# Kernel tuning notes

Hardware: AMD Instinct MI355X
Metric: run time of the kernel (lower is better)

Reference implementation:

```python
import jax, jax.numpy as jnp
import numpy as np

N, C, H, W = 2, 8, 256, 512
K = 9   # kernel_size
D = 1   # dilation


def setup_inputs() -> dict:
    key = jax.random.key(0)
    k1, k2, k3 = jax.random.split(key, 3)
    x_in = jax.random.normal(k1, (N, C, H, W), dtype=jnp.float32)
    filters = jax.random.normal(k2, (N, K * K, H, W), dtype=jnp.float32)
    filters_biases = jax.random.normal(k3, (N, 1, H, W), dtype=jnp.float32)
    return {"x_in": x_in, "filters": filters, "filters_biases": filters_biases}


def reference(x_in, filters, filters_biases):
    # Dynamic (per-pixel) filtering: out[n,c,h,w] = sum_{i,j} x_pad[n,c,h+i*d,w+j*d] * filters[n,i*K+j,h,w] + bias
    # Equivalent to torch: unfold -> [N,C,K*K,H,W], multiply by filters [N,1,K*K,H,W], sum over K*K, add bias.
    # Fused accumulation over the K*K taps avoids materializing the K*K-times larger im2col tensor.
    k, d = K, D
    p = d * (k - 1) // 2  # 'same' padding used by im2col_layer
    n, c, h, w = x_in.shape
    xp = jnp.pad(x_in, ((0, 0), (0, 0), (p, p), (p, p)))
    out = jnp.zeros_like(x_in)
    for i in range(k):          # fixed small kernel loop (81 taps), unrolled by jit
        for j in range(k):
            tap = filters[:, None, i * k + j]                  # [N,1,H,W]
            out = out + xp[:, :, i * d:i * d + h, j * d:j * d + w] * tap
    return out + filters_biases
```

## Files before the change

### kernel.cpp

```cpp
#include <hip/hip_runtime.h>

#define CC 8
#define HH 256
#define WW 512
#define KK 9
#define XS_STRIDE 532

__global__ __launch_bounds__(256) void dynfilter_kernel(
    const float* __restrict__ x,
    const float* __restrict__ filt,
    const float* __restrict__ fbias,
    float* __restrict__ out)
{
    __shared__ __align__(16) float xs[CC][XS_STRIDE];

    const int tid = threadIdx.x;
    const int bid = blockIdx.x;
    const int n = bid >> 8;
    const int h = bid & 255;
    const int w0 = tid << 1;

    const int lane32 = tid & 31;
    const int cstage = tid >> 5;

    float acc0[CC], acc1[CC];
    {
        const float2 fb = *(const float2*)(fbias + (n * HH + h) * WW + w0);
        #pragma unroll
        for (int c = 0; c < CC; ++c) { acc0[c] = fb.x; acc1[c] = fb.y; }
    }

    const float* xcbase = x + ((size_t)(n * CC + cstage)) * HH * WW;

    for (int i = 0; i < KK; ++i) {
        const int hh = h + i - 4;
        const bool rowok = (hh >= 0) && (hh < HH);

        __syncthreads();
        const float4* src = (const float4*)(xcbase + hh * WW);
        #pragma unroll
        for (int it = 0; it < 5; ++it) {
            const int k = lane32 + (it << 5);
            if (k < 130) {
                const int w = (k << 2) - 4;
                float4 v = make_float4(0.f, 0.f, 0.f, 0.f);
                if (rowok && (unsigned)w < (unsigned)WW) v = src[w >> 2];
                *(float4*)&xs[cstage][w + 4] = v;
            }
        }
        __syncthreads();

        const float* frow = filt + ((size_t)(n * 81 + i * KK) * HH + h) * WW + w0;
        float2 fr[KK];
        #pragma unroll
        for (int j = 0; j < KK; ++j)
            fr[j] = *(const float2*)(frow + (size_t)j * (HH * WW));

        #pragma unroll
        for (int c = 0; c < CC; ++c) {
            float xr[10];
            #pragma unroll
            for (int s = 0; s < 5; ++s)
                *(float2*)&xr[2 * s] = *(const float2*)&xs[c][w0 + 2 * s];
            #pragma unroll
            for (int j = 0; j < KK; ++j) {
                acc0[c] = fmaf(fr[j].x, xr[j],     acc0[c]);
                acc1[c] = fmaf(fr[j].y, xr[j + 1], acc1[c]);
            }
        }
    }

    #pragma unroll
    for (int c = 0; c < CC; ++c) {
        *(float2*)(out + ((size_t)(n * CC + c) * HH + h) * WW + w0) =
            make_float2(acc0[c], acc1[c]);
    }
}

extern "C" void kernel_launch(void* const* d_in, const int* in_sizes, int n_in,
                              void* d_out, int out_size, void* d_ws, size_t ws_size,
                              hipStream_t stream) {
    const float* x  = (const float*)d_in[0];
    const float* f  = (const float*)d_in[1];
    const float* fb = (const float*)d_in[2];
    float* o = (float*)d_out;
    hipLaunchKernelGGL(dynfilter_kernel, dim3(2 * HH), dim3(256), 0, stream,
                       x, f, fb, o);
}
```

Baseline: 156.3 us.

## Split rows into segments, remap threads to pixels×channel-pairs, double-buffer LDS

Each image row is now split into two 256-pixel segments, which doubles the grid. Each thread now computes 4 pixels for 2 channels instead of 2 pixels for 8 channels. The input rows are double-buffered in shared memory, and the next tap row is prefetched into registers while the current one is being computed, so each tap row needs a single barrier. The aim is more blocks in flight and load latency hidden behind FMAs. The cost is that each filter value is now loaded by four channel-pair thread groups instead of one, which adds cache traffic.

```diff
diff --git a/kernel.cpp b/kernel.cpp
--- a/kernel.cpp
+++ b/kernel.cpp
@@ -4,76 +4,104 @@
 #define HH 256
 #define WW 512
 #define KK 9
-#define XS_STRIDE 532
+#define SEGW 256
+#define XF 272
 
-__global__ __launch_bounds__(256) void dynfilter_kernel(
+__global__ __launch_bounds__(256, 4) void dynfilter_kernel(
     const float* __restrict__ x,
     const float* __restrict__ filt,
     const float* __restrict__ fbias,
     float* __restrict__ out)
 {
-    __shared__ __align__(16) float xs[CC][XS_STRIDE];
+    __shared__ __align__(16) float xs[2][CC][XF];
 
     const int tid = threadIdx.x;
     const int bid = blockIdx.x;
-    const int n = bid >> 8;
-    const int h = bid & 255;
-    const int w0 = tid << 1;
+    const int seg = bid & 1;
+    const int h   = (bid >> 1) & 255;
+    const int n   = bid >> 9;
+
+    const int pxg = tid & 63;
+    const int cp  = tid >> 6;
+    const int w0  = seg * SEGW + (pxg << 2);
+    const int c0  = cp << 1;
 
     const int lane32 = tid & 31;
     const int cstage = tid >> 5;
+    const float* xrowbase = x + ((size_t)(n * CC + cstage)) * (HH * WW)
+                              + (seg * SEGW - 8);
+    const int wbase = seg * SEGW - 8;
 
-    float acc0[CC], acc1[CC];
+    float acc[2][4];
     {
-        const float2 fb = *(const float2*)(fbias + (n * HH + h) * WW + w0);
+        const float4 fb = *(const float4*)(fbias + ((size_t)(n * HH + h)) * WW + w0);
         #pragma unroll
-        for (int c = 0; c < CC; ++c) { acc0[c] = fb.x; acc1[c] = fb.y; }
-    }
-
-    const float* xcbase = x + ((size_t)(n * CC + cstage)) * HH * WW;
-
-    for (int i = 0; i < KK; ++i) {
-        const int hh = h + i - 4;
-        const bool rowok = (hh >= 0) && (hh < HH);
-
-        __syncthreads();
-        const float4* src = (const float4*)(xcbase + hh * WW);
-        #pragma unroll
-        for (int it = 0; it < 5; ++it) {
-            const int k = lane32 + (it << 5);
-            if (k < 130) {
-                const int w = (k << 2) - 4;
-                float4 v = make_float4(0.f, 0.f, 0.f, 0.f);
-                if (rowok && (unsigned)w < (unsigned)WW) v = src[w >> 2];
-                *(float4*)&xs[cstage][w + 4] = v;
-            }
-        }
-        __syncthreads();
-
-        const float* frow = filt + ((size_t)(n * 81 + i * KK) * HH + h) * WW + w0;
-        float2 fr[KK];
-        #pragma unroll
-        for (int j = 0; j < KK; ++j)
-            fr[j] = *(const float2*)(frow + (size_t)j * (HH * WW));
-
-        #pragma unroll
-        for (int c = 0; c < CC; ++c) {
-            float xr[10];
-            #pragma unroll
-            for (int s = 0; s < 5; ++s)
-                *(float2*)&xr[2 * s] = *(const float2*)&xs[c][w0 + 2 * s];
-            #pragma unroll
-            for (int j = 0; j < KK; ++j) {
-                acc0[c] = fmaf(fr[j].x, xr[j],     acc0[c]);
-                acc1[c] = fmaf(fr[j].y, xr[j + 1], acc1[c]);
-            }
+        for (int cc = 0; cc < 2; ++cc) {
+            acc[cc][0] = fb.x; acc[cc][1] = fb.y; acc[cc][2] = fb.z; acc[cc][3] = fb.w;
         }
     }
 
+    float4 xv[3];
+    auto issue_stage = [&](int hh) {
+        const bool rowok = (unsigned)hh < (unsigned)HH;
+        const float* src = xrowbase + (size_t)hh * WW;
+        #pragma unroll
+        for (int r = 0; r < 3; ++r) {
+            const int k = lane32 + (r << 5);
+            const int wg = wbase + (k << 2);
+            xv[r] = make_float4(0.f, 0.f, 0.f, 0.f);
+            if (k < 68 && rowok && (unsigned)wg < (unsigned)WW)
+                xv[r] = *(const float4*)(src + (k << 2));
+        }
+    };
+    auto store_stage = [&](int buf) {
+        #pragma unroll
+        for (int r = 0; r < 3; ++r) {
+            const int k = lane32 + (r << 5);
+            if (k < 68) *(float4*)&xs[buf][cstage][k << 2] = xv[r];
+        }
+    };
+
+    issue_stage(h - 4);
+    store_stage(0);
+    __syncthreads();
+
+    const size_t HW = (size_t)HH * WW;
+    const float* fbase = filt + ((size_t)(n * 81) * HH + h) * WW + w0;
+
     #pragma unroll
-    for (int c = 0; c < CC; ++c) {
-        *(float2*)(out + ((size_t)(n * CC + c) * HH + h) * WW + w0) =
-            make_float2(acc0[c], acc1[c]);
+    for (int i = 0; i < KK; ++i) {
+        float4 fr[KK];
+        #pragma unroll
+        for (int j = 0; j < KK; ++j)
+            fr[j] = *(const float4*)(fbase + (size_t)(i * KK + j) * HW);
+
+        if (i < KK - 1) issue_stage(h - 4 + i + 1);
+
+        #pragma unroll
+        for (int cc = 0; cc < 2; ++cc) {
+            const float* xr = &xs[i & 1][c0 + cc][(pxg << 2) + 4];
+            float xf[12];
+            *(float4*)&xf[0] = *(const float4*)&xr[0];
+            *(float4*)&xf[4] = *(const float4*)&xr[4];
+            *(float4*)&xf[8] = *(const float4*)&xr[8];
+            #pragma unroll
+            for (int j = 0; j < KK; ++j) {
+                acc[cc][0] = fmaf(fr[j].x, xf[j],     acc[cc][0]);
+                acc[cc][1] = fmaf(fr[j].y, xf[j + 1], acc[cc][1]);
+                acc[cc][2] = fmaf(fr[j].z, xf[j + 2], acc[cc][2]);
+                acc[cc][3] = fmaf(fr[j].w, xf[j + 3], acc[cc][3]);
+            }
+        }
+
+        if (i < KK - 1) store_stage((i + 1) & 1);
+        __syncthreads();
+    }
+
+    #pragma unroll
+    for (int cc = 0; cc < 2; ++cc) {
+        *(float4*)(out + ((size_t)(n * CC + c0 + cc) * HH + h) * WW + w0) =
+            make_float4(acc[cc][0], acc[cc][1], acc[cc][2], acc[cc][3]);
     }
 }
 
@@ -84,6 +112,6 @@
     const float* f  = (const float*)d_in[1];
     const float* fb = (const float*)d_in[2];
     float* o = (float*)d_out;
-    hipLaunchKernelGGL(dynfilter_kernel, dim3(2 * HH), dim3(256), 0, stream,
+    hipLaunchKernelGGL(dynfilter_kernel, dim3(2 * HH * 2), dim3(256), 0, stream,
                        x, f, fb, o);
 }
```

Measured after the change: 382.1 us. 144% more time.

## Split rows into half-width segments, split channels across threads, double-buffer LDS rows

Applied to the files above, without the earlier changes.

Each block now covers half a row: 1024 blocks instead of 512, and each thread computes 4 channels for 2 pixels instead of 8 channels. The x row staging is double-buffered in shared memory, so the next row's global loads are issued before the FMAs on the current row, and there is one barrier per tap row instead of two. The goal is more parallelism and occupancy, plus overlap of load latency with compute. The cost is that filter taps are now loaded twice per pixel, once for each channel group, and each block stages some redundant halo.

```diff
diff --git a/kernel.cpp b/kernel.cpp
--- a/kernel.cpp
+++ b/kernel.cpp
@@ -4,76 +4,111 @@
 #define HH 256
 #define WW 512
 #define KK 9
-#define XS_STRIDE 532
+#define XF 268
 
-__global__ __launch_bounds__(256) void dynfilter_kernel(
+__global__ __launch_bounds__(256, 4) void dynfilter_kernel(
     const float* __restrict__ x,
     const float* __restrict__ filt,
     const float* __restrict__ fbias,
     float* __restrict__ out)
 {
-    __shared__ __align__(16) float xs[CC][XS_STRIDE];
+    __shared__ __align__(16) float xs[2][CC][XF];
 
     const int tid = threadIdx.x;
     const int bid = blockIdx.x;
-    const int n = bid >> 8;
-    const int h = bid & 255;
-    const int w0 = tid << 1;
+    const int seg = bid & 1;
+    const int h   = (bid >> 1) & 255;
+    const int n   = bid >> 9;
 
-    const int lane32 = tid & 31;
-    const int cstage = tid >> 5;
+    const int pxg = tid & 127;
+    const int cg  = tid >> 7;
+    const int w0  = seg * 256 + (pxg << 1);
 
-    float acc0[CC], acc1[CC];
+    const int lane32  = tid & 31;
+    const int cstage  = tid >> 5;
+    const int wstage0 = seg * 256 - 4;
+    const float* xcrow = x + ((size_t)(n * CC + cstage)) * ((size_t)HH * WW) + wstage0;
+
+    const size_t HW = (size_t)HH * WW;
+    const float* fbase = filt + ((size_t)(n * 81) * HH + h) * WW + w0;
+
+    float acc[4][2];
     {
-        const float2 fb = *(const float2*)(fbias + (n * HH + h) * WW + w0);
+        const float2 fb = *(const float2*)(fbias + ((size_t)(n * HH + h)) * WW + w0);
         #pragma unroll
-        for (int c = 0; c < CC; ++c) { acc0[c] = fb.x; acc1[c] = fb.y; }
+        for (int c = 0; c < 4; ++c) { acc[c][0] = fb.x; acc[c][1] = fb.y; }
     }
 
-    const float* xcbase = x + ((size_t)(n * CC + cstage)) * HH * WW;
+    {
+        const int hh = h - 4;
+        const bool rowok = (hh >= 0);
+        const float* src = xcrow + (size_t)hh * WW;
+        float4 s0 = make_float4(0.f,0.f,0.f,0.f), s1 = s0, s2 = s0;
+        int w;
+        w = wstage0 + (lane32 << 2);
+        if (rowok && (unsigned)w < (unsigned)WW) s0 = *(const float4*)(src + (lane32 << 2));
+        w = wstage0 + ((lane32 + 32) << 2);
+        if (rowok && (unsigned)w < (unsigned)WW) s1 = *(const float4*)(src + ((lane32 + 32) << 2));
+        w = wstage0 + ((lane32 + 64) << 2);
+        if (lane32 < 2 && rowok && (unsigned)w < (unsigned)WW) s2 = *(const float4*)(src + ((lane32 + 64) << 2));
+        *(float4*)&xs[0][cstage][lane32 << 2] = s0;
+        *(float4*)&xs[0][cstage][(lane32 + 32) << 2] = s1;
+        if (lane32 < 2) *(float4*)&xs[0][cstage][(lane32 + 64) << 2] = s2;
+    }
+    __syncthreads();
 
+    #pragma unroll
     for (int i = 0; i < KK; ++i) {
-        const int hh = h + i - 4;
-        const bool rowok = (hh >= 0) && (hh < HH);
+        const int buf = i & 1;
 
-        __syncthreads();
-        const float4* src = (const float4*)(xcbase + hh * WW);
+        float2 f[KK];
         #pragma unroll
-        for (int it = 0; it < 5; ++it) {
-            const int k = lane32 + (it << 5);
-            if (k < 130) {
-                const int w = (k << 2) - 4;
-                float4 v = make_float4(0.f, 0.f, 0.f, 0.f);
-                if (rowok && (unsigned)w < (unsigned)WW) v = src[w >> 2];
-                *(float4*)&xs[cstage][w + 4] = v;
+        for (int j = 0; j < KK; ++j)
+            f[j] = *(const float2*)(fbase + (size_t)(i * KK + j) * HW);
+
+        float4 s0 = make_float4(0.f,0.f,0.f,0.f), s1 = s0, s2 = s0;
+        if (i < KK - 1) {
+            const int hh = h - 4 + i + 1;
+            const bool rowok = (unsigned)hh < (unsigned)HH;
+            const float* src = xcrow + (size_t)hh * WW;
+            int w;
+            w = wstage0 + (lane32 << 2);
+            if (rowok && (unsigned)w < (unsigned)WW) s0 = *(const float4*)(src + (lane32 << 2));
+            w = wstage0 + ((lane32 + 32) << 2);
+            if (rowok && (unsigned)w < (unsigned)WW) s1 = *(const float4*)(src + ((lane32 + 32) << 2));
+            w = wstage0 + ((lane32 + 64) << 2);
+            if (lane32 < 2 && rowok && (unsigned)w < (unsigned)WW) s2 = *(const float4*)(src + ((lane32 + 64) << 2));
+        }
+
+        #pragma unroll
+        for (int c = 0; c < 4; ++c) {
+            const float* xp = &xs[buf][(cg << 2) + c][pxg << 1];
+            float xr[10];
+            float2 v;
+            v = *(const float2*)(xp + 0); xr[0] = v.x; xr[1] = v.y;
+            v = *(const float2*)(xp + 2); xr[2] = v.x; xr[3] = v.y;
+            v = *(const float2*)(xp + 4); xr[4] = v.x; xr[5] = v.y;
+            v = *(const float2*)(xp + 6); xr[6] = v.x; xr[7] = v.y;
+            v = *(const float2*)(xp + 8); xr[8] = v.x; xr[9] = v.y;
+            #pragma unroll
+            for (int j = 0; j < KK; ++j) {
+                acc[c][0] = fmaf(f[j].x, xr[j],     acc[c][0]);
+                acc[c][1] = fmaf(f[j].y, xr[j + 1], acc[c][1]);
             }
         }
+
+        if (i < KK - 1) {
+            *(float4*)&xs[buf ^ 1][cstage][lane32 << 2] = s0;
+            *(float4*)&xs[buf ^ 1][cstage][(lane32 + 32) << 2] = s1;
+            if (lane32 < 2) *(float4*)&xs[buf ^ 1][cstage][(lane32 + 64) << 2] = s2;
+        }
         __syncthreads();
-
-        const float* frow = filt + ((size_t)(n * 81 + i * KK) * HH + h) * WW + w0;
-        float2 fr[KK];
-        #pragma unroll
-        for (int j = 0; j < KK; ++j)
-            fr[j] = *(const float2*)(frow + (size_t)j * (HH * WW));
-
-        #pragma unroll
-        for (int c = 0; c < CC; ++c) {
-            float xr[10];
-            #pragma unroll
-            for (int s = 0; s < 5; ++s)
-                *(float2*)&xr[2 * s] = *(const float2*)&xs[c][w0 + 2 * s];
-            #pragma unroll
-            for (int j = 0; j < KK; ++j) {
-                acc0[c] = fmaf(fr[j].x, xr[j],     acc0[c]);
-                acc1[c] = fmaf(fr[j].y, xr[j + 1], acc1[c]);
-            }
-        }
     }
 
     #pragma unroll
-    for (int c = 0; c < CC; ++c) {
-        *(float2*)(out + ((size_t)(n * CC + c) * HH + h) * WW + w0) =
-            make_float2(acc0[c], acc1[c]);
+    for (int c = 0; c < 4; ++c) {
+        *(float2*)(out + ((size_t)(n * CC + (cg << 2) + c) * HH + h) * WW + w0) =
+            make_float2(acc[c][0], acc[c][1]);
     }
 }
 
@@ -84,6 +119,6 @@
     const float* f  = (const float*)d_in[1];
     const float* fb = (const float*)d_in[2];
     float* o = (float*)d_out;
-    hipLaunchKernelGGL(dynfilter_kernel, dim3(2 * HH), dim3(256), 0, stream,
+    hipLaunchKernelGGL(dynfilter_kernel, dim3(1024), dim3(256), 0, stream,
                        x, f, fb, o);
 }
```

New measurement: 433.9 us. 178% more time.

## Split rows into width segments, stage all 9 input rows upfront, prefetch filter taps

Applied to the files above, without the earlier changes.

Each block now handles a 128-wide segment of one row instead of the full row, so the grid grows fourfold. Each thread computes 2 channels × 2 pixels instead of 8 channels × 2 pixels. All 9 halo rows for 8 channels are loaded into shared memory once with a single barrier, replacing the per-row sync loop. Filter taps for the next kernel row are register-prefetched to overlap global latency with FMAs. The trade-off is that each filter value is now read by 4 thread groups (one per channel pair) instead of once, which raises L2/global filter traffic, while occupancy and parallelism improve.

```diff
diff --git a/kernel.cpp b/kernel.cpp
--- a/kernel.cpp
+++ b/kernel.cpp
@@ -4,7 +4,8 @@
 #define HH 256
 #define WW 512
 #define KK 9
-#define XS_STRIDE 532
+#define SEGW 128
+#define XROW 136
 
 __global__ __launch_bounds__(256) void dynfilter_kernel(
     const float* __restrict__ x,
@@ -12,69 +13,120 @@
     const float* __restrict__ fbias,
     float* __restrict__ out)
 {
-    __shared__ __align__(16) float xs[CC][XS_STRIDE];
+    __shared__ __align__(16) float xs[KK][CC][XROW];
 
     const int tid = threadIdx.x;
     const int bid = blockIdx.x;
-    const int n = bid >> 8;
-    const int h = bid & 255;
-    const int w0 = tid << 1;
+    const int seg = bid & 3;
+    const int h   = (bid >> 2) & 255;
+    const int n   = bid >> 10;
+
+    const int pxg = tid & 63;
+    const int cgr = tid >> 6;
+    const int c0  = cgr << 1;
+    const int w0  = seg * SEGW + (pxg << 1);
 
     const int lane32 = tid & 31;
     const int cstage = tid >> 5;
+    const size_t HW = (size_t)HH * WW;
+    const float* xc = x + ((size_t)(n * CC + cstage)) * HW;
 
-    float acc0[CC], acc1[CC];
     {
-        const float2 fb = *(const float2*)(fbias + (n * HH + h) * WW + w0);
-        #pragma unroll
-        for (int c = 0; c < CC; ++c) { acc0[c] = fb.x; acc1[c] = fb.y; }
-    }
-
-    const float* xcbase = x + ((size_t)(n * CC + cstage)) * HH * WW;
-
-    for (int i = 0; i < KK; ++i) {
-        const int hh = h + i - 4;
-        const bool rowok = (hh >= 0) && (hh < HH);
-
-        __syncthreads();
-        const float4* src = (const float4*)(xcbase + hh * WW);
-        #pragma unroll
-        for (int it = 0; it < 5; ++it) {
-            const int k = lane32 + (it << 5);
-            if (k < 130) {
-                const int w = (k << 2) - 4;
-                float4 v = make_float4(0.f, 0.f, 0.f, 0.f);
-                if (rowok && (unsigned)w < (unsigned)WW) v = src[w >> 2];
-                *(float4*)&xs[cstage][w + 4] = v;
-            }
-        }
-        __syncthreads();
-
-        const float* frow = filt + ((size_t)(n * 81 + i * KK) * HH + h) * WW + w0;
-        float2 fr[KK];
-        #pragma unroll
-        for (int j = 0; j < KK; ++j)
-            fr[j] = *(const float2*)(frow + (size_t)j * (HH * WW));
-
-        #pragma unroll
-        for (int c = 0; c < CC; ++c) {
-            float xr[10];
-            #pragma unroll
-            for (int s = 0; s < 5; ++s)
-                *(float2*)&xr[2 * s] = *(const float2*)&xs[c][w0 + 2 * s];
-            #pragma unroll
-            for (int j = 0; j < KK; ++j) {
-                acc0[c] = fmaf(fr[j].x, xr[j],     acc0[c]);
-                acc1[c] = fmaf(fr[j].y, xr[j + 1], acc1[c]);
-            }
+        const int wbody = seg * SEGW + (lane32 << 2);
+        const int whalo = (lane32 == 0) ? (seg * SEGW - 4) : (seg * SEGW + SEGW);
+        const int ihalo = (lane32 == 0) ? 0 : (XROW - 4);
+        for (int r = 0; r < KK; ++r) {
+            const int hh = h + r - 4;
+            const bool rowok = (unsigned)hh < (unsigned)HH;
+            const float* src = xc + (size_t)hh * WW;
+            float4 sb = make_float4(0.f, 0.f, 0.f, 0.f);
+            float4 sh = sb;
+            if (rowok) sb = *(const float4*)(src + wbody);
+            if (lane32 < 2 && rowok && (unsigned)whalo < (unsigned)WW)
+                sh = *(const float4*)(src + whalo);
+            *(float4*)&xs[r][cstage][4 + (lane32 << 2)] = sb;
+            if (lane32 < 2) *(float4*)&xs[r][cstage][ihalo] = sh;
         }
     }
 
-    #pragma unroll
-    for (int c = 0; c < CC; ++c) {
-        *(float2*)(out + ((size_t)(n * CC + c) * HH + h) * WW + w0) =
-            make_float2(acc0[c], acc1[c]);
+    const float* fptr = filt + ((size_t)(n * 81) * HH + h) * WW + w0;
+
+    float a00, a01, a10, a11;
+    {
+        const float2 fb = *(const float2*)(fbias + ((size_t)(n * HH + h)) * WW + w0);
+        a00 = fb.x; a01 = fb.y; a10 = fb.x; a11 = fb.y;
     }
+
+    float2 f0 = *(const float2*)(fptr + 0 * HW);
+    float2 f1 = *(const float2*)(fptr + 1 * HW);
+    float2 f2 = *(const float2*)(fptr + 2 * HW);
+    float2 f3 = *(const float2*)(fptr + 3 * HW);
+    float2 f4 = *(const float2*)(fptr + 4 * HW);
+    float2 f5 = *(const float2*)(fptr + 5 * HW);
+    float2 f6 = *(const float2*)(fptr + 6 * HW);
+    float2 f7 = *(const float2*)(fptr + 7 * HW);
+    float2 f8 = *(const float2*)(fptr + 8 * HW);
+
+    __syncthreads();
+
+    #pragma clang loop unroll(disable)
+    for (int i = 0; i < KK; ++i) {
+        float2 g0, g1, g2, g3, g4, g5, g6, g7, g8;
+        g0 = g1 = g2 = g3 = g4 = g5 = g6 = g7 = g8 = make_float2(0.f, 0.f);
+        if (i < KK - 1) {
+            const float* fi = fptr + (size_t)(i + 1) * KK * HW;
+            g0 = *(const float2*)(fi + 0 * HW);
+            g1 = *(const float2*)(fi + 1 * HW);
+            g2 = *(const float2*)(fi + 2 * HW);
+            g3 = *(const float2*)(fi + 3 * HW);
+            g4 = *(const float2*)(fi + 4 * HW);
+            g5 = *(const float2*)(fi + 5 * HW);
+            g6 = *(const float2*)(fi + 6 * HW);
+            g7 = *(const float2*)(fi + 7 * HW);
+            g8 = *(const float2*)(fi + 8 * HW);
+        }
+
+        {
+            const float* xp = &xs[i][c0][pxg << 1];
+            float2 v0 = *(const float2*)(xp + 0);
+            float2 v1 = *(const float2*)(xp + 2);
+            float2 v2 = *(const float2*)(xp + 4);
+            float2 v3 = *(const float2*)(xp + 6);
+            float2 v4 = *(const float2*)(xp + 8);
+            a00 = fmaf(f0.x, v0.x, a00);  a01 = fmaf(f0.y, v0.y, a01);
+            a00 = fmaf(f1.x, v0.y, a00);  a01 = fmaf(f1.y, v1.x, a01);
+            a00 = fmaf(f2.x, v1.x, a00);  a01 = fmaf(f2.y, v1.y, a01);
+            a00 = fmaf(f3.x, v1.y, a00);  a01 = fmaf(f3.y, v2.x, a01);
+            a00 = fmaf(f4.x, v2.x, a00);  a01 = fmaf(f4.y, v2.y, a01);
+            a00 = fmaf(f5.x, v2.y, a00);  a01 = fmaf(f5.y, v3.x, a01);
+            a00 = fmaf(f6.x, v3.x, a00);  a01 = fmaf(f6.y, v3.y, a01);
+            a00 = fmaf(f7.x, v3.y, a00);  a01 = fmaf(f7.y, v4.x, a01);
+            a00 = fmaf(f8.x, v4.x, a00);  a01 = fmaf(f8.y, v4.y, a01);
+        }
+        {
+            const float* xp = &xs[i][c0 + 1][pxg << 1];
+            float2 v0 = *(const float2*)(xp + 0);
+            float2 v1 = *(const float2*)(xp + 2);
+            float2 v2 = *(const float2*)(xp + 4);
+            float2 v3 = *(const float2*)(xp + 6);
+            float2 v4 = *(const float2*)(xp + 8);
+            a10 = fmaf(f0.x, v0.x, a10);  a11 = fmaf(f0.y, v0.y, a11);
+            a10 = fmaf(f1.x, v0.y, a10);  a11 = fmaf(f1.y, v1.x, a11);
+            a10 = fmaf(f2.x, v1.x, a10);  a11 = fmaf(f2.y, v1.y, a11);
+            a10 = fmaf(f3.x, v1.y, a10);  a11 = fmaf(f3.y, v2.x, a11);
+            a10 = fmaf(f4.x, v2.x, a10);  a11 = fmaf(f4.y, v2.y, a11);
+            a10 = fmaf(f5.x, v2.y, a10);  a11 = fmaf(f5.y, v3.x, a11);
+            a10 = fmaf(f6.x, v3.x, a10);  a11 = fmaf(f6.y, v3.y, a11);
+            a10 = fmaf(f7.x, v3.y, a10);  a11 = fmaf(f7.y, v4.x, a11);
+            a10 = fmaf(f8.x, v4.x, a10);  a11 = fmaf(f8.y, v4.y, a11);
+        }
+
+        f0 = g0; f1 = g1; f2 = g2; f3 = g3; f4 = g4;
+        f5 = g5; f6 = g6; f7 = g7; f8 = g8;
+    }
+
+    *(float2*)(out + ((size_t)(n * CC + c0) * HH + h) * WW + w0) = make_float2(a00, a01);
+    *(float2*)(out + ((size_t)(n * CC + c0 + 1) * HH + h) * WW + w0) = make_float2(a10, a11);
 }
 
 extern "C" void kernel_launch(void* const* d_in, const int* in_sizes, int n_in,
@@ -84,6 +136,6 @@
     const float* f  = (const float*)d_in[1];
     const float* fb = (const float*)d_in[2];
     float* o = (float*)d_out;
-    hipLaunchKernelGGL(dynfilter_kernel, dim3(2 * HH), dim3(256), 0, stream,
+    hipLaunchKernelGGL(dynfilter_kernel, dim3(2048), dim3(256), 0, stream,
                        x, f, fb, o);
 }
```

New measurement: 153.5 us. About the same (-1.8%).
